# Performance work log

Measured on AMD Instinct MI355X. Metric: run time of the kernel, lower is better.

The kernel has to match this reference:

```python
import jax, jax.numpy as jnp
import numpy as np

A_BITS = 4          # a_bits
W_BITS = 4          # w_bits / w_slices (w_slices = 1)
NUM_CHUNKS = 9      # ceil(in_ch*9 / 64) = ceil(576/64)
BN_EPS = 1e-5


def quantize_weight(w, bits):
    # WeightQuantize STE: uniform symmetric quantization, straight-through on clipped range
    n = 2.0 ** (bits - 1) - 1.0
    c = jnp.clip(w, -1.0, 1.0)
    q = jnp.round(c * n) / n
    return c + jax.lax.stop_gradient(q - c)


def create_input_stream(a, a_bits):
    # residual multi-bit binarization into a_bits sign planes, x ~= sum_i plane_i / 2^(i+1)
    x = jnp.clip(a, -1.0, 1.0)
    planes = []
    r = x
    for i in range(a_bits):
        s = jnp.where(r >= 0, 1.0, -1.0)
        planes.append(x + jax.lax.stop_gradient(s - x))  # STE plane
        r = r - s / (2.0 ** (i + 1))
    return jnp.stack(planes, 0)  # [a_bits, B, C*9, L]


def unfold3x3(x, pad=1):
    # torch F.unfold(kernel=3, stride=1) ordering: (C, kh, kw) flattened channel-major
    B, C, H, W = x.shape
    xp = jnp.pad(x, ((0, 0), (0, 0), (pad, pad), (pad, pad)))
    cols = jnp.stack([xp[:, :, i:i + H, j:j + W] for i in range(3) for j in range(3)], axis=2)
    return cols.reshape(B, C * 9, H * W)  # [B, C*9, L]


def mtj(x, gamma, beta, key):
    mean = x.mean(axis=(0, 2), keepdims=True)
    var = x.var(axis=(0, 2), keepdims=True)  # biased, as torch BN
    normed = (x - mean) / jnp.sqrt(var + BN_EPS) * gamma[None, :, None] + beta[None, :, None]
    t = jnp.tanh(4.0 * normed)
    rand = jax.random.uniform(key, x.shape, minval=-1.0, maxval=1.0)
    out = jnp.where(t > rand, 1.0, -1.0)
    out = jnp.where(normed == 0.0, 0.0, out)
    c = jnp.clip(normed, -1.0, 1.0)
    return c + jax.lax.stop_gradient(out - c)


def setup_inputs() -> dict:
    key = jax.random.key(0)
    k1, k2 = jax.random.split(key)
    inputs = jax.random.normal(k1, (8, 64, 32, 32), dtype=jnp.float32)
    weight = jax.random.normal(k2, (128, 64, 3, 3), dtype=jnp.float32) * (2.0 / (64 * 9)) ** 0.5
    gamma = jnp.ones((128,), jnp.float32)
    beta = jnp.zeros((128,), jnp.float32)
    return {"inputs": inputs, "weight": weight, "gamma": gamma, "beta": beta}


def reference(inputs, weight, gamma, beta):
    O = weight.shape[0]
    # weight standardization (per output filter; std is unbiased as torch .std())
    wf = weight.reshape(O, -1)
    bw = weight - wf.mean(-1)[:, None, None, None]
    std = bw.reshape(O, -1).std(-1, ddof=1)
    bw = bw / std[:, None, None, None]
    qw = quantize_weight(bw, W_BITS)                      # [O, C, 3, 3]
    a = unfold3x3(inputs)                                 # [B, C*9, L]
    stream = create_input_stream(a, A_BITS)               # [A, B, C*9, L]
    A, B, CK, L = stream.shape
    cs = CK // NUM_CHUNKS
    x = stream.reshape(A * B, NUM_CHUNKS, cs, L)          # chunked along the C*9 axis
    fw = qw.reshape(O, NUM_CHUNKS, cs)                    # flattened weight chunks
    # per-chunk F.linear, vectorized over chunks: [nc, A*B, O, L]
    lt = jnp.einsum('ngkl,ogk->gnol', x, fw)
    keys = jax.random.split(jax.random.key(42), NUM_CHUNKS)
    pre = jax.vmap(lambda t, k: mtj(t, gamma, beta, k))(lt, keys) / NUM_CHUNKS
    out = pre.sum(0)                                      # sum chunks (w_slices=1 -> identity combine)
    # gen_image_vector_and_sum: recombine activation bit-planes
    out = out.reshape(A, B, O, L)
    wts = (2.0 ** -(jnp.arange(A, dtype=jnp.float32) + 1.0)).reshape(A, 1, 1, 1)
    out = (out * wts).sum(0)
    HW = int(np.sqrt(L))
    return out.reshape(B, O, HW, HW)                      # F.fold with (1,1) kernel
```

## Files before the change

kernel.cpp:

```cpp
#include <hip/hip_runtime.h>
#include <stdint.h>

#ifndef PRNG_PARTITIONABLE
#define PRNG_PARTITIONABLE 1
#endif

#define ONE_M_U 0.99999994039535522461f

__device__ __forceinline__ void tf_4a(uint32_t& x0, uint32_t& x1){
  x0 += x1; x1 = (x1<<13)|(x1>>19); x1 ^= x0;
  x0 += x1; x1 = (x1<<15)|(x1>>17); x1 ^= x0;
  x0 += x1; x1 = (x1<<26)|(x1>>6);  x1 ^= x0;
  x0 += x1; x1 = (x1<<6) |(x1>>26); x1 ^= x0;
}
__device__ __forceinline__ void tf_4b(uint32_t& x0, uint32_t& x1){
  x0 += x1; x1 = (x1<<17)|(x1>>15); x1 ^= x0;
  x0 += x1; x1 = (x1<<29)|(x1>>3);  x1 ^= x0;
  x0 += x1; x1 = (x1<<16)|(x1>>16); x1 ^= x0;
  x0 += x1; x1 = (x1<<24)|(x1>>8);  x1 ^= x0;
}
__device__ __forceinline__ void threefry2x32(uint32_t k0, uint32_t k1, uint32_t& x0, uint32_t& x1){
  uint32_t k2 = k0 ^ k1 ^ 0x1BD11BDAu;
  x0 += k0; x1 += k1;
  tf_4a(x0,x1); x0 += k1; x1 += k2 + 1u;
  tf_4b(x0,x1); x0 += k2; x1 += k0 + 2u;
  tf_4a(x0,x1); x0 += k0; x1 += k1 + 3u;
  tf_4b(x0,x1); x0 += k1; x1 += k2 + 4u;
  tf_4a(x0,x1); x0 += k2; x1 += k0 + 5u;
}

__device__ __forceinline__ float bits_to_unit(uint32_t b){
  #pragma clang fp contract(off)
  float f = __uint_as_float((b >> 9) | 0x3f800000u) - 1.0f;
  float r = f * 2.0f + (-1.0f);
  return __builtin_fmaxf(-1.0f, r);
}

__device__ __forceinline__ float xla_tanh_f32(float x){
  #pragma clang fp contract(off)
  float ax = __builtin_fabsf(x);
  float xc = __builtin_fminf(__builtin_fmaxf(x, -9.0f), 9.0f);
  float x2 = xc * xc;
  float nm = -2.76076847742355e-16f;
  nm = x2 * nm + 2.00018790482477e-13f;
  nm = x2 * nm + -8.60467152213735e-11f;
  nm = x2 * nm + 5.12229709037114e-08f;
  nm = x2 * nm + 1.48572235717979e-05f;
  nm = x2 * nm + 6.37261928875436e-04f;
  nm = x2 * nm + 4.89352455891786e-03f;
  nm = xc * nm;
  float dn = 1.19825839466702e-06f;
  dn = x2 * dn + 1.18534705686654e-04f;
  dn = x2 * dn + 2.26843463243900e-03f;
  dn = x2 * dn + 4.89352518554385e-03f;
  float res = nm / dn;
  return (ax < 0.0004f) ? x : res;
}

__device__ __forceinline__ float dot64(unsigned long long sw, unsigned long long dw,
                                       const float* w){
  float acc = 0.0f;
  #pragma unroll
  for (int k = 0; k < 64; ++k){
    float mag = ((dw >> k) & 1ull) ? ONE_M_U : 1.0f;
    float p   = ((sw >> k) & 1ull) ? mag : -mag;
    acc = __builtin_fmaf(p, w[k], acc);
  }
  return acc;
}

#define QW_OFF   0u
#define SGN_OFF  294912u
#define DIM_OFF  2654208u
#define KEYS_OFF 5013504u
#define MV_OFF   5013632u
#define LT_OFF   5023744u
#define LT_BYTES 150994944u
#define PART_OFF  (LT_OFF + LT_BYTES)
#define PART_BYTES 2359296u
#define PART2_OFF (PART_OFF + PART_BYTES)
#define WS_NEEDED_FAST (PART2_OFF + PART_BYTES)

__global__ __launch_bounds__(256) void k_front(const float* __restrict__ X,
        const float* __restrict__ W, float* __restrict__ qw, uint32_t* __restrict__ keys,
        unsigned long long* __restrict__ sgn, unsigned long long* __restrict__ dimw){
  #pragma clang fp contract(off)
  __shared__ float  bwL[576];
  __shared__ double red[64];
  int bx = blockIdx.x;
  int t = threadIdx.x;
  if (bx < 288){
    int g = bx >> 5;
    int tid = (bx & 31) * 256 + t;
    int b = tid >> 10, l = tid & 1023;
    int h = l >> 5, w = l & 31;
    unsigned long long sw0=0ull, sw1=0ull, sw2=0ull, sw3=0ull;
    unsigned long long dw0=0ull, dw1=0ull, dw2=0ull, dw3=0ull;
    const float* Xb = X + b*64*1024;
    int ck0 = g*64;
    #pragma unroll
    for (int i = 0; i < 64; ++i){
      int ck = ck0 + i;
      int c = ck / 9, kp = ck % 9;
      int di = kp / 3 - 1, dj = kp % 3 - 1;
      int hh = h + di, ww = w + dj;
      float v = 0.0f;
      if (hh >= 0 && hh < 32 && ww >= 0 && ww < 32)
        v = Xb[(c*32 + hh)*32 + ww];
      float x = __builtin_fminf(__builtin_fmaxf(v, -1.0f), 1.0f);
      float r = x;
      {
        float sv = (r >= 0.0f) ? 1.0f : -1.0f;
        float d  = sv - x; float p = x + d;
        if (sv > 0.0f) sw0 |= (1ull << i);
        if (__builtin_fabsf(p) < 1.0f) dw0 |= (1ull << i);
        r = r - sv * 0.5f;
      }
      {
        float sv = (r >= 0.0f) ? 1.0f : -1.0f;
        float d  = sv - x; float p = x + d;
        if (sv > 0.0f) sw1 |= (1ull << i);
        if (__builtin_fabsf(p) < 1.0f) dw1 |= (1ull << i);
        r = r - sv * 0.25f;
      }
      {
        float sv = (r >= 0.0f) ? 1.0f : -1.0f;
        float d  = sv - x; float p = x + d;
        if (sv > 0.0f) sw2 |= (1ull << i);
        if (__builtin_fabsf(p) < 1.0f) dw2 |= (1ull << i);
        r = r - sv * 0.125f;
      }
      {
        float sv = (r >= 0.0f) ? 1.0f : -1.0f;
        float d  = sv - x; float p = x + d;
        if (sv > 0.0f) sw3 |= (1ull << i);
        if (__builtin_fabsf(p) < 1.0f) dw3 |= (1ull << i);
        r = r - sv * 0.0625f;
      }
    }
    sgn [((0*8+b)*9 + g)*1024 + l] = sw0;
    sgn [((1*8+b)*9 + g)*1024 + l] = sw1;
    sgn [((2*8+b)*9 + g)*1024 + l] = sw2;
    sgn [((3*8+b)*9 + g)*1024 + l] = sw3;
    dimw[((0*8+b)*9 + g)*1024 + l] = dw0;
    dimw[((1*8+b)*9 + g)*1024 + l] = dw1;
    dimw[((2*8+b)*9 + g)*1024 + l] = dw2;
    dimw[((3*8+b)*9 + g)*1024 + l] = dw3;
  } else {
    int o = bx - 288;
    if (t < 64){
      double s = 0.0;
      for (int j = t; j < 576; j += 64) s += (double)W[o*576 + j];
      red[t] = s;
    }
    __syncthreads();
    for (int k = 32; k > 0; k >>= 1){ if (t < k) red[t] += red[t+k]; __syncthreads(); }
    float mean1 = (float)(red[0] / 576.0);
    __syncthreads();
    for (int j = t; j < 576; j += 256) bwL[j] = W[o*576 + j] - mean1;
    __syncthreads();
    if (t < 64){
      double s = 0.0;
      for (int j = t; j < 576; j += 64) s += (double)bwL[j];
      red[t] = s;
    }
    __syncthreads();
    for (int k = 32; k > 0; k >>= 1){ if (t < k) red[t] += red[t+k]; __syncthreads(); }
    float mean2 = (float)(red[0] / 576.0);
    __syncthreads();
    if (t < 64){
      double s = 0.0;
      for (int j = t; j < 576; j += 64){ float c = bwL[j] - mean2; float sq = c * c; s += (double)sq; }
      red[t] = s;
    }
    __syncthreads();
    for (int k = 32; k > 0; k >>= 1){ if (t < k) red[t] += red[t+k]; __syncthreads(); }
    float varf = (float)(red[0] / 575.0);
    float stdv = __builtin_sqrtf(varf);
    __syncthreads();
    for (int j = t; j < 576; j += 256){
      float b2 = bwL[j] / stdv;
      float c  = __builtin_fminf(__builtin_fmaxf(b2, -1.0f), 1.0f);
      float q  = __builtin_rintf(c * 7.0f) / 7.0f;
      float fwd = c + (q - c);
      int g = j >> 6, k = j & 63;
      qw [(g*128 + o)*64 + k] = fwd;
    }
    if (o == 0 && t == 0){
#if PRNG_PARTITIONABLE
      for (int g = 0; g < 9; ++g){
        uint32_t x0 = 0u, x1 = (uint32_t)g;
        threefry2x32(0u, 42u, x0, x1);
        keys[2*g] = x0; keys[2*g+1] = x1;
      }
#else
      uint32_t outv[18];
      for (int i = 0; i < 9; ++i){
        uint32_t x0 = (uint32_t)i, x1 = (uint32_t)(9 + i);
        threefry2x32(0u, 42u, x0, x1);
        outv[i] = x0; outv[9+i] = x1;
      }
      for (int j = 0; j < 18; ++j) keys[j] = outv[j];
#endif
    }
  }
}

__global__ __launch_bounds__(256, 3) void k_gemm(const float* __restrict__ qw,
        const unsigned long long* __restrict__ sgn, const unsigned long long* __restrict__ dimw,
        float* __restrict__ lt, double* __restrict__ part, double* __restrict__ part2){
  __shared__ float4 wS[128*17];
  __shared__ float4 pS[128*9];
  int lq = blockIdx.x, g = blockIdx.y, n = blockIdx.z;
  int t = threadIdx.x;
  {
    int o = t >> 4, kq = t & 15;
    const float4* qw4 = (const float4*)qw;
    #pragma unroll
    for (int i = 0; i < 8; ++i){
      int oo = o + 16*i;
      wS[oo*17 + kq] = qw4[(g*128 + oo)*16 + kq];
    }
  }
  int lde = t >> 1, kh = t & 1;
  unsigned long long sw = sgn [(n*9+g)*1024 + lq*128 + lde];
  unsigned long long dw = dimw[(n*9+g)*1024 + lq*128 + lde];
  int ot = t >> 4, ltl = t & 15;
  float acc[8][8];
  #pragma unroll
  for (int i = 0; i < 8; ++i)
    #pragma unroll
    for (int j = 0; j < 8; ++j) acc[i][j] = 0.0f;
  #pragma unroll
  for (int h = 0; h < 2; ++h){
    #pragma unroll
    for (int q = 0; q < 4; ++q){
      int kq2 = kh*4 + q;
      int k = (h*8 + kq2)*4;
      float4 v;
      float m0 = ((dw>>k)&1ull)?ONE_M_U:1.0f;     v.x = ((sw>>k)&1ull)?m0:-m0;
      float m1 = ((dw>>(k+1))&1ull)?ONE_M_U:1.0f; v.y = ((sw>>(k+1))&1ull)?m1:-m1;
      float m2 = ((dw>>(k+2))&1ull)?ONE_M_U:1.0f; v.z = ((sw>>(k+2))&1ull)?m2:-m2;
      float m3 = ((dw>>(k+3))&1ull)?ONE_M_U:1.0f; v.w = ((sw>>(k+3))&1ull)?m3:-m3;
      pS[lde*9 + kq2] = v;
    }
    __syncthreads();
    for (int kq2 = 0; kq2 < 8; ++kq2){
      int kq = h*8 + kq2;
      float wr[8][4], pr[8][4];
      #pragma unroll
      for (int i = 0; i < 8; ++i) *(float4*)wr[i] = wS[(ot*8+i)*17 + kq];
      #pragma unroll
      for (int j = 0; j < 8; ++j) *(float4*)pr[j] = pS[(ltl+16*j)*9 + kq2];
      #pragma unroll
      for (int e = 0; e < 4; ++e)
        #pragma unroll
        for (int i = 0; i < 8; ++i)
          #pragma unroll
          for (int j = 0; j < 8; ++j)
            acc[i][j] = __builtin_fmaf(pr[j][e], wr[i][e], acc[i][j]);
    }
    __syncthreads();
  }
  #pragma unroll
  for (int i = 0; i < 8; ++i){
    int o = ot*8 + i;
    float* dst = lt + ((size_t)((n*9+g)*128 + o))*1024 + lq*128 + ltl;
    #pragma unroll
    for (int j = 0; j < 8; ++j) dst[16*j] = acc[i][j];
  }
  double ps1[8], ps2[8];
  #pragma unroll
  for (int i = 0; i < 8; ++i){
    double s1 = 0.0, s2 = 0.0;
    #pragma unroll
    for (int j = 0; j < 8; ++j){
      double d = (double)acc[i][j];
      s1 += d;
      s2 += d * d;
    }
    ps1[i] = s1; ps2[i] = s2;
  }
  double* red = (double*)pS;
  #pragma unroll
  for (int i = 0; i < 8; ++i) red[(ot*8+i)*16 + ltl] = ps1[i];
  __syncthreads();
  if (t < 128){
    double s = 0.0;
    #pragma unroll
    for (int q = 0; q < 16; ++q) s += red[t*16 + q];
    part[((size_t)g*128 + t)*256 + n*8 + lq] = s;
  }
  __syncthreads();
  #pragma unroll
  for (int i = 0; i < 8; ++i) red[(ot*8+i)*16 + ltl] = ps2[i];
  __syncthreads();
  if (t < 128){
    double s = 0.0;
    #pragma unroll
    for (int q = 0; q < 16; ++q) s += red[t*16 + q];
    part2[((size_t)g*128 + t)*256 + n*8 + lq] = s;
  }
}

__global__ __launch_bounds__(64) void k_den(const double* __restrict__ part,
        const double* __restrict__ part2, float* __restrict__ mv){
  __shared__ double redm[64];
  __shared__ double redv[64];
  int go = blockIdx.x, t = threadIdx.x;
  double s = 0.0;
  for (int idx = t; idx < 256; idx += 64) s += part[(size_t)go*256 + idx];
  redm[t] = s;
  double v = 0.0;
  for (int idx = t; idx < 256; idx += 64) v += part2[(size_t)go*256 + idx];
  redv[t] = v;
  __syncthreads();
  for (int k = 32; k > 0; k >>= 1){
    if (t < k){ redm[t] += redm[t+k]; redv[t] += redv[t+k]; }
    __syncthreads();
  }
  if (t == 0){
    float mean = (float)(redm[0] / 32768.0);
    mv[go*2] = mean;
    double m = (double)mean;
    double var64 = (redv[0] - 2.0*m*redm[0] + 32768.0*m*m) / 32768.0;
    float varf = (float)var64;
    mv[go*2 + 1] = __builtin_sqrtf(varf + 1e-5f);
  }
}

__global__ __launch_bounds__(256) void k_out_fast(const float* __restrict__ lt,
        const float* __restrict__ mv, const uint32_t* __restrict__ keys,
        const float* __restrict__ gamma, const float* __restrict__ beta,
        float* __restrict__ out){
  #pragma clang fp contract(off)
  __shared__ float    mvL[18];
  __shared__ uint32_t kL[18];
  int bi = blockIdx.x;
  int lc = bi & 3, o = (bi >> 2) & 127, b = bi >> 9;
  int t = threadIdx.x;
  if (t < 18){ mvL[t] = mv[((t>>1)*128 + o)*2 + (t&1)]; kL[t] = keys[t]; }
  __syncthreads();
  int l = lc*256 + t;
  float gma = gamma[o], bta = beta[o];
  float S[4] = {0.0f, 0.0f, 0.0f, 0.0f};
  for (int g = 0; g < 9; ++g){
    float rnd[4];
#if PRNG_PARTITIONABLE
    #pragma unroll
    for (int a = 0; a < 4; ++a){
      uint32_t m = (uint32_t)((a*8 + b)*131072 + o*1024 + l);
      uint32_t x0 = 0u, x1 = m;
      threefry2x32(kL[2*g], kL[2*g+1], x0, x1);
      rnd[a] = bits_to_unit(x0 ^ x1);
    }
#else
    #pragma unroll
    for (int a01 = 0; a01 < 2; ++a01){
      uint32_t m = (uint32_t)((a01*8 + b)*131072 + o*1024 + l);
      uint32_t x0 = m, x1 = m + 2097152u;
      threefry2x32(kL[2*g], kL[2*g+1], x0, x1);
      rnd[a01]     = bits_to_unit(x0);
      rnd[a01 + 2] = bits_to_unit(x1);
    }
#endif
    float mean = mvL[2*g], den = mvL[2*g+1];
    #pragma unroll
    for (int a = 0; a < 4; ++a){
      int n = a*8 + b;
      float tv = lt[((size_t)((n*9+g)*128 + o)) * 1024 + l];
      float normed = (tv - mean) / den * gma + bta;
      float th = xla_tanh_f32(4.0f * normed);
      float dec = (th > rnd[a]) ? 1.0f : -1.0f;
      if (normed == 0.0f) dec = 0.0f;
      float cc  = __builtin_fminf(__builtin_fmaxf(normed, -1.0f), 1.0f);
      float fwd = cc + (dec - cc);
      float pre = fwd / 9.0f;
      S[a] = S[a] + pre;
    }
  }
  float z = S[0] * 0.5f;
  z = z + S[1] * 0.25f;
  z = z + S[2] * 0.125f;
  z = z + S[3] * 0.0625f;
  out[(b*128 + o)*1024 + l] = z;
}

__global__ __launch_bounds__(256) void k_stats_slow(const float* __restrict__ qw,
        const unsigned long long* __restrict__ sgn, const unsigned long long* __restrict__ dimw,
        float* __restrict__ mv){
  #pragma clang fp contract(off)
  __shared__ double red[256];
  int g = blockIdx.x >> 7, o = blockIdx.x & 127, t = threadIdx.x;
  float wr[64];
  #pragma unroll
  for (int k = 0; k < 64; ++k) wr[k] = qw[(g*128 + o)*64 + k];
  double s1 = 0.0;
  for (int n = 0; n < 32; ++n){
    const unsigned long long* sp = sgn  + (n*9 + g)*1024;
    const unsigned long long* dp = dimw + (n*9 + g)*1024;
    for (int j = 0; j < 4; ++j){
      int l = t + j*256;
      float tvv = dot64(sp[l], dp[l], wr);
      s1 += (double)tvv;
    }
  }
  red[t] = s1; __syncthreads();
  for (int k = 128; k > 0; k >>= 1){ if (t < k) red[t] += red[t+k]; __syncthreads(); }
  float mean = (float)(red[0] / 32768.0);
  __syncthreads();
  double s2 = 0.0;
  for (int n = 0; n < 32; ++n){
    const unsigned long long* sp = sgn  + (n*9 + g)*1024;
    const unsigned long long* dp = dimw + (n*9 + g)*1024;
    for (int j = 0; j < 4; ++j){
      int l = t + j*256;
      float tvv = dot64(sp[l], dp[l], wr);
      float c = tvv - mean;
      float sq = c * c;
      s2 += (double)sq;
    }
  }
  red[t] = s2; __syncthreads();
  for (int k = 128; k > 0; k >>= 1){ if (t < k) red[t] += red[t+k]; __syncthreads(); }
  if (t == 0){
    float var = (float)(red[0] / 32768.0);
    float den = __builtin_sqrtf(var + 1e-5f);
    mv[(g*128+o)*2]   = mean;
    mv[(g*128+o)*2+1] = den;
  }
}

__global__ __launch_bounds__(256) void k_out_slow(const float* __restrict__ qw,
        const unsigned long long* __restrict__ sgn, const unsigned long long* __restrict__ dimw,
        const float* __restrict__ mv, const uint32_t* __restrict__ keys,
        const float* __restrict__ gamma, const float* __restrict__ beta,
        float* __restrict__ out){
  #pragma clang fp contract(off)
  __shared__ float    wv[576];
  __shared__ float    mvL[18];
  __shared__ uint32_t kL[18];
  int bi = blockIdx.x;
  int lc = bi & 3, o = (bi >> 2) & 127, b = bi >> 9;
  int t = threadIdx.x;
  for (int j = t; j < 576; j += 256) wv[j] = qw[((j >> 6)*128 + o)*64 + (j & 63)];
  if (t < 18){ mvL[t] = mv[((t>>1)*128 + o)*2 + (t&1)]; kL[t] = keys[t]; }
  __syncthreads();
  int l = lc*256 + t;
  float gma = gamma[o], bta = beta[o];
  float S[4] = {0.0f, 0.0f, 0.0f, 0.0f};
  for (int g = 0; g < 9; ++g){
    float rnd[4];
#if PRNG_PARTITIONABLE
    #pragma unroll
    for (int a = 0; a < 4; ++a){
      uint32_t m = (uint32_t)((a*8 + b)*131072 + o*1024 + l);
      uint32_t x0 = 0u, x1 = m;
      threefry2x32(kL[2*g], kL[2*g+1], x0, x1);
      rnd[a] = bits_to_unit(x0 ^ x1);
    }
#else
    #pragma unroll
    for (int a01 = 0; a01 < 2; ++a01){
      uint32_t m = (uint32_t)((a01*8 + b)*131072 + o*1024 + l);
      uint32_t x0 = m, x1 = m + 2097152u;
      threefry2x32(kL[2*g], kL[2*g+1], x0, x1);
      rnd[a01]     = bits_to_unit(x0);
      rnd[a01 + 2] = bits_to_unit(x1);
    }
#endif
    float mean = mvL[2*g], den = mvL[2*g+1];
    float wr[64];
    #pragma unroll
    for (int k = 0; k < 64; ++k) wr[k] = wv[g*64 + k];
    #pragma unroll
    for (int a = 0; a < 4; ++a){
      int n = a*8 + b;
      float tvv = dot64(sgn[(n*9+g)*1024 + l], dimw[(n*9+g)*1024 + l], wr);
      float normed = (tvv - mean) / den * gma + bta;
      float th = xla_tanh_f32(4.0f * normed);
      float dec = (th > rnd[a]) ? 1.0f : -1.0f;
      if (normed == 0.0f) dec = 0.0f;
      float cc  = __builtin_fminf(__builtin_fmaxf(normed, -1.0f), 1.0f);
      float fwd = cc + (dec - cc);
      float pre = fwd / 9.0f;
      S[a] = S[a] + pre;
    }
  }
  float z = S[0] * 0.5f;
  z = z + S[1] * 0.25f;
  z = z + S[2] * 0.125f;
  z = z + S[3] * 0.0625f;
  out[(b*128 + o)*1024 + l] = z;
}

extern "C" void kernel_launch(void* const* d_in, const int* in_sizes, int n_in,
                              void* d_out, int out_size, void* d_ws, size_t ws_size,
                              hipStream_t stream){
  (void)in_sizes; (void)n_in; (void)out_size;
  const float* inp   = (const float*)d_in[0];
  const float* wgt   = (const float*)d_in[1];
  const float* gamma = (const float*)d_in[2];
  const float* beta  = (const float*)d_in[3];
  float* out = (float*)d_out;
  char* ws = (char*)d_ws;
  float*              qw    = (float*)(ws + QW_OFF);
  unsigned long long* sgn   = (unsigned long long*)(ws + SGN_OFF);
  unsigned long long* dimw  = (unsigned long long*)(ws + DIM_OFF);
  uint32_t*           keys  = (uint32_t*)(ws + KEYS_OFF);
  float*              mv    = (float*)(ws + MV_OFF);
  float*              lt    = (float*)(ws + LT_OFF);
  double*             part  = (double*)(ws + PART_OFF);
  double*             part2 = (double*)(ws + PART2_OFF);

  hipLaunchKernelGGL(k_front, dim3(416), dim3(256), 0, stream, inp, wgt, qw, keys, sgn, dimw);
  if (ws_size >= (size_t)WS_NEEDED_FAST){
    hipLaunchKernelGGL(k_gemm,     dim3(8, 9, 32), dim3(256), 0, stream, qw, sgn, dimw,
                       lt, part, part2);
    hipLaunchKernelGGL(k_den,      dim3(1152),     dim3(64),  0, stream, part, part2, mv);
    hipLaunchKernelGGL(k_out_fast, dim3(4096),     dim3(256), 0, stream, lt, mv, keys,
                       gamma, beta, out);
  } else {
    hipLaunchKernelGGL(k_stats_slow, dim3(1152), dim3(256), 0, stream, qw, sgn, dimw, mv);
    hipLaunchKernelGGL(k_out_slow,   dim3(4096), dim3(256), 0, stream, qw, sgn, dimw, mv, keys,
                       gamma, beta, out);
  }
}
```

Before: 273.9 us.

## Process two batch-plane slices per GEMM block to reuse staged weight tile

Each k_gemm block now loops over two n slices, loading the weight chunk into shared memory once and reusing it for both. The activation tile is expanded to a full 16-quad stride so one staging pass covers the whole K range and the inner loop drops the half split. The grid z dimension is halved and the occupancy hint in launch_bounds is removed. This cuts redundant weight loads and block count, at the cost of larger shared memory per block, fewer blocks in flight, and a serial dependency between the two slices.

```diff
diff --git a/kernel.cpp b/kernel.cpp
--- a/kernel.cpp
+++ b/kernel.cpp
@@ -206,12 +206,12 @@
   }
 }
 
-__global__ __launch_bounds__(256, 3) void k_gemm(const float* __restrict__ qw,
+__global__ __launch_bounds__(256) void k_gemm(const float* __restrict__ qw,
         const unsigned long long* __restrict__ sgn, const unsigned long long* __restrict__ dimw,
         float* __restrict__ lt, double* __restrict__ part, double* __restrict__ part2){
   __shared__ float4 wS[128*17];
-  __shared__ float4 pS[128*9];
-  int lq = blockIdx.x, g = blockIdx.y, n = blockIdx.z;
+  __shared__ float4 pS[128*17];
+  int lq = blockIdx.x, g = blockIdx.y, nz = blockIdx.z;
   int t = threadIdx.x;
   {
     int o = t >> 4, kq = t & 15;
@@ -222,36 +222,40 @@
       wS[oo*17 + kq] = qw4[(g*128 + oo)*16 + kq];
     }
   }
-  int lde = t >> 1, kh = t & 1;
-  unsigned long long sw = sgn [(n*9+g)*1024 + lq*128 + lde];
-  unsigned long long dw = dimw[(n*9+g)*1024 + lq*128 + lde];
   int ot = t >> 4, ltl = t & 15;
-  float acc[8][8];
-  #pragma unroll
-  for (int i = 0; i < 8; ++i)
-    #pragma unroll
-    for (int j = 0; j < 8; ++j) acc[i][j] = 0.0f;
-  #pragma unroll
-  for (int h = 0; h < 2; ++h){
-    #pragma unroll
-    for (int q = 0; q < 4; ++q){
-      int kq2 = kh*4 + q;
-      int k = (h*8 + kq2)*4;
-      float4 v;
-      float m0 = ((dw>>k)&1ull)?ONE_M_U:1.0f;     v.x = ((sw>>k)&1ull)?m0:-m0;
-      float m1 = ((dw>>(k+1))&1ull)?ONE_M_U:1.0f; v.y = ((sw>>(k+1))&1ull)?m1:-m1;
-      float m2 = ((dw>>(k+2))&1ull)?ONE_M_U:1.0f; v.z = ((sw>>(k+2))&1ull)?m2:-m2;
-      float m3 = ((dw>>(k+3))&1ull)?ONE_M_U:1.0f; v.w = ((sw>>(k+3))&1ull)?m3:-m3;
-      pS[lde*9 + kq2] = v;
-    }
-    __syncthreads();
-    for (int kq2 = 0; kq2 < 8; ++kq2){
-      int kq = h*8 + kq2;
+  for (int n2 = 0; n2 < 2; ++n2){
+    int n = nz*2 + n2;
+    if (n2) __syncthreads();
+    {
+      int l = t >> 1, kh = t & 1;
+      unsigned long long sw = sgn [(n*9+g)*1024 + lq*128 + l];
+      unsigned long long dw = dimw[(n*9+g)*1024 + lq*128 + l];
+      #pragma unroll
+      for (int kq = 0; kq < 8; ++kq){
+        int kqq = kh*8 + kq;
+        float4 v;
+        {
+          int k = kqq*4;
+          float m0 = ((dw>>k)&1ull)?ONE_M_U:1.0f;     v.x = ((sw>>k)&1ull)?m0:-m0;
+          float m1 = ((dw>>(k+1))&1ull)?ONE_M_U:1.0f; v.y = ((sw>>(k+1))&1ull)?m1:-m1;
+          float m2 = ((dw>>(k+2))&1ull)?ONE_M_U:1.0f; v.z = ((sw>>(k+2))&1ull)?m2:-m2;
+          float m3 = ((dw>>(k+3))&1ull)?ONE_M_U:1.0f; v.w = ((sw>>(k+3))&1ull)?m3:-m3;
+        }
+        pS[l*17 + kqq] = v;
+      }
+    }
+    __syncthreads();
+    float acc[8][8];
+    #pragma unroll
+    for (int i = 0; i < 8; ++i)
+      #pragma unroll
+      for (int j = 0; j < 8; ++j) acc[i][j] = 0.0f;
+    for (int kq = 0; kq < 16; ++kq){
       float wr[8][4], pr[8][4];
       #pragma unroll
       for (int i = 0; i < 8; ++i) *(float4*)wr[i] = wS[(ot*8+i)*17 + kq];
       #pragma unroll
-      for (int j = 0; j < 8; ++j) *(float4*)pr[j] = pS[(ltl+16*j)*9 + kq2];
+      for (int j = 0; j < 8; ++j) *(float4*)pr[j] = pS[(ltl+16*j)*17 + kq];
       #pragma unroll
       for (int e = 0; e < 4; ++e)
         #pragma unroll
@@ -260,46 +264,46 @@
           for (int j = 0; j < 8; ++j)
             acc[i][j] = __builtin_fmaf(pr[j][e], wr[i][e], acc[i][j]);
     }
-    __syncthreads();
-  }
-  #pragma unroll
-  for (int i = 0; i < 8; ++i){
-    int o = ot*8 + i;
-    float* dst = lt + ((size_t)((n*9+g)*128 + o))*1024 + lq*128 + ltl;
-    #pragma unroll
-    for (int j = 0; j < 8; ++j) dst[16*j] = acc[i][j];
-  }
-  double ps1[8], ps2[8];
-  #pragma unroll
-  for (int i = 0; i < 8; ++i){
-    double s1 = 0.0, s2 = 0.0;
-    #pragma unroll
-    for (int j = 0; j < 8; ++j){
-      double d = (double)acc[i][j];
-      s1 += d;
-      s2 += d * d;
-    }
-    ps1[i] = s1; ps2[i] = s2;
-  }
-  double* red = (double*)pS;
-  #pragma unroll
-  for (int i = 0; i < 8; ++i) red[(ot*8+i)*16 + ltl] = ps1[i];
-  __syncthreads();
-  if (t < 128){
-    double s = 0.0;
-    #pragma unroll
-    for (int q = 0; q < 16; ++q) s += red[t*16 + q];
-    part[((size_t)g*128 + t)*256 + n*8 + lq] = s;
-  }
-  __syncthreads();
-  #pragma unroll
-  for (int i = 0; i < 8; ++i) red[(ot*8+i)*16 + ltl] = ps2[i];
-  __syncthreads();
-  if (t < 128){
-    double s = 0.0;
-    #pragma unroll
-    for (int q = 0; q < 16; ++q) s += red[t*16 + q];
-    part2[((size_t)g*128 + t)*256 + n*8 + lq] = s;
+    #pragma unroll
+    for (int i = 0; i < 8; ++i){
+      int o = ot*8 + i;
+      float* dst = lt + ((size_t)((n*9+g)*128 + o))*1024 + lq*128 + ltl;
+      #pragma unroll
+      for (int j = 0; j < 8; ++j) dst[16*j] = acc[i][j];
+    }
+    double ps1[8], ps2[8];
+    #pragma unroll
+    for (int i = 0; i < 8; ++i){
+      double s1 = 0.0, s2 = 0.0;
+      #pragma unroll
+      for (int j = 0; j < 8; ++j){
+        double d = (double)acc[i][j];
+        s1 += d;
+        s2 += d * d;
+      }
+      ps1[i] = s1; ps2[i] = s2;
+    }
+    __syncthreads();
+    double* red = (double*)pS;
+    #pragma unroll
+    for (int i = 0; i < 8; ++i) red[(ot*8+i)*16 + ltl] = ps1[i];
+    __syncthreads();
+    if (t < 128){
+      double s = 0.0;
+      #pragma unroll
+      for (int q = 0; q < 16; ++q) s += red[t*16 + q];
+      part[((size_t)g*128 + t)*256 + n*8 + lq] = s;
+    }
+    __syncthreads();
+    #pragma unroll
+    for (int i = 0; i < 8; ++i) red[(ot*8+i)*16 + ltl] = ps2[i];
+    __syncthreads();
+    if (t < 128){
+      double s = 0.0;
+      #pragma unroll
+      for (int q = 0; q < 16; ++q) s += red[t*16 + q];
+      part2[((size_t)g*128 + t)*256 + n*8 + lq] = s;
+    }
   }
 }
 
@@ -515,7 +519,7 @@
 
   hipLaunchKernelGGL(k_front, dim3(416), dim3(256), 0, stream, inp, wgt, qw, keys, sgn, dimw);
   if (ws_size >= (size_t)WS_NEEDED_FAST){
-    hipLaunchKernelGGL(k_gemm,     dim3(8, 9, 32), dim3(256), 0, stream, qw, sgn, dimw,
+    hipLaunchKernelGGL(k_gemm,     dim3(8, 9, 16), dim3(256), 0, stream, qw, sgn, dimw,
                        lt, part, part2);
     hipLaunchKernelGGL(k_den,      dim3(1152),     dim3(64),  0, stream, part, part2, mv);
     hipLaunchKernelGGL(k_out_fast, dim3(4096),     dim3(256), 0, stream, lt, mv, keys,
```

Result: no change. 275.9 us (+0.7%).
